# Kernel tuning notes

Measured on AMD Instinct MI355X. Metric: run time of the kernel, lower is better.

## Reference

```python
import jax, jax.numpy as jnp
import numpy as np

N = 2048
E = 512
H = 8
DH = E // H
L = 2
MAX_DIST = 10
LOCAL_DIST = 2
NUM_COLORS = 16
NEG_INF = -1e9


def _layer_norm(x, scale, bias, eps=1e-5):
    mu = jnp.mean(x, axis=-1, keepdims=True)
    var = jnp.mean(jnp.square(x - mu), axis=-1, keepdims=True)
    return (x - mu) * jax.lax.rsqrt(var + eps) * scale + bias


def setup_inputs() -> dict:
    key = jax.random.key(0)
    ks = jax.random.split(key, 12)
    s = 0.05  # weight init scale for numerical sanity
    return {
        "D": jax.random.randint(ks[0], (N, N), 0, MAX_DIST + 2, dtype=jnp.int32),
        "x": jax.random.normal(ks[1], (1, N, E), dtype=jnp.float32),
        "dist_emb": jax.random.normal(ks[2], (MAX_DIST + 2, 8), dtype=jnp.float32) * s,
        "dist_proj_w": jax.random.normal(ks[3], (1, 8), dtype=jnp.float32) * s,
        "dist_proj_b": jnp.zeros((1,), jnp.float32),
        "ln1_scale": jnp.ones((L, E), jnp.float32),
        "ln1_bias": jnp.zeros((L, E), jnp.float32),
        "in_proj_w": jax.random.normal(ks[4], (L, 3 * E, E), dtype=jnp.float32) * s,
        "in_proj_b": jnp.zeros((L, 3 * E), jnp.float32),
        "out_w": jax.random.normal(ks[5], (L, E, E), dtype=jnp.float32) * s,
        "out_b": jnp.zeros((L, E), jnp.float32),
        "ln2_scale": jnp.ones((L, E), jnp.float32),
        "ln2_bias": jnp.zeros((L, E), jnp.float32),
        "ff1_w": jax.random.normal(ks[6], (L, 2 * E, E), dtype=jnp.float32) * s,
        "ff1_b": jnp.zeros((L, 2 * E), jnp.float32),
        "ff2_w": jax.random.normal(ks[7], (L, E, 2 * E), dtype=jnp.float32) * s,
        "ff2_b": jnp.zeros((L, E), jnp.float32),
        "color_w": jax.random.normal(ks[8], (NUM_COLORS, E), dtype=jnp.float32) * s,
        "color_b": jnp.zeros((NUM_COLORS,), jnp.float32),
    }


def reference(D, x, dist_emb, dist_proj_w, dist_proj_b,
              ln1_scale, ln1_bias, in_proj_w, in_proj_b, out_w, out_b,
              ln2_scale, ln2_bias, ff1_w, ff1_b, ff2_w, ff2_b,
              color_w, color_b):
    # Distance encoder: clamp -> embed -> project to scalar bias per (i, j)
    d_clamped = jnp.clip(D, 0, MAX_DIST + 1)                        # [N, N]
    emb = dist_emb[d_clamped]                                       # [N, N, 8]
    bias = jnp.einsum('nme,e->nm', emb, dist_proj_w[0]) + dist_proj_b[0]
    # Graph-local sparsity: real bias within local_dist, -inf elsewhere
    attn_mask = jnp.where(D <= LOCAL_DIST, bias, NEG_INF)           # [N, N]

    scale = 1.0 / jnp.sqrt(jnp.asarray(DH, x.dtype))
    for l in range(L):
        # --- pre-norm multihead self-attention ---
        xn = _layer_norm(x, ln1_scale[l], ln1_bias[l])              # [1, N, E]
        qkv = jnp.einsum('bne,fe->bnf', xn, in_proj_w[l]) + in_proj_b[l]
        q, k, v = jnp.split(qkv, 3, axis=-1)                        # each [1, N, E]
        q = q.reshape(1, N, H, DH)
        k = k.reshape(1, N, H, DH)
        v = v.reshape(1, N, H, DH)
        scores = jnp.einsum('bnhd,bmhd->bhnm', q, k) * scale        # [1, H, N, N]
        scores = scores + attn_mask[None, None, :, :]
        probs = jax.nn.softmax(scores, axis=-1)
        attn = jnp.einsum('bhnm,bmhd->bnhd', probs, v).reshape(1, N, E)
        attn = jnp.einsum('bne,fe->bnf', attn, out_w[l]) + out_b[l]
        x = x + attn                                                # dropout = identity (eval)
        # --- pre-norm feed-forward ---
        xf = _layer_norm(x, ln2_scale[l], ln2_bias[l])
        h = jax.nn.relu(jnp.einsum('bne,fe->bnf', xf, ff1_w[l]) + ff1_b[l])
        ff = jnp.einsum('bnf,ef->bne', h, ff2_w[l]) + ff2_b[l]
        x = x + ff

    logits = jnp.einsum('bne,ce->bnc', x, color_w) + color_b        # [1, N, C]
    return jax.nn.softmax(logits, axis=-1)[0]                       # [N, C]
```

## Files before the change

kernel.cpp:

```cpp
#include <hip/hip_runtime.h>
#include <cstddef>
#include <cstdint>

#define NN 2048
#define EE 512
#define HH 8
#define QKVF 1536
#define NSEG 4

typedef __attribute__((ext_vector_type(4))) float f32x4;
typedef __attribute__((ext_vector_type(8))) short s16x8;
typedef __attribute__((ext_vector_type(4))) short s16x4;

static __device__ __forceinline__ unsigned short f2bf(float x) {
  union { float f; unsigned int u; } c; c.f = x;
  unsigned int r = (c.u + 0x7FFFu + ((c.u >> 16) & 1u)) >> 16;
  return (unsigned short)r;
}
static __device__ __forceinline__ float bf2f(unsigned short b) {
  union { unsigned int u; float f; } c; c.u = ((unsigned int)b) << 16;
  return c.f;
}

#define GLL16(gp, lp) __builtin_amdgcn_global_load_lds( \
    (const __attribute__((address_space(1))) void*)(gp), \
    (__attribute__((address_space(3))) void*)(lp), 16, 0, 0)

__global__ __launch_bounds__(256) void cvt_bf4(const float* __restrict__ src,
    unsigned short* __restrict__ dst, int n4) {
  int i = blockIdx.x * 256 + threadIdx.x;
  if (i < n4) {
    float4 v = ((const float4*)src)[i];
    s16x4 o;
    o[0] = (short)f2bf(v.x); o[1] = (short)f2bf(v.y);
    o[2] = (short)f2bf(v.z); o[3] = (short)f2bf(v.w);
    ((s16x4*)dst)[i] = o;
  }
}

__global__ void wtbl_kernel(const float* __restrict__ demb, const float* __restrict__ dpw,
    const float* __restrict__ dpb, float* __restrict__ wtbl) {
  int t = threadIdx.x;
  if (t < 4) {
    float v = 0.f;
    if (t < 3) {
      float s = 0.f;
      for (int e = 0; e < 8; e++) s += demb[t * 8 + e] * dpw[e];
      v = expf(s + dpb[0]);
    }
    wtbl[t] = v;
  }
}

__global__ __launch_bounds__(256) void mask_pack(const int* __restrict__ D,
    unsigned int* __restrict__ codes) {
  int id = blockIdx.x * 256 + threadIdx.x;
  int row = id >> 9;
  int u = id & 511;
  int ch = u >> 4, col = u & 15;
  int base = ch * 64 + col;
  unsigned int pk = 0;
#pragma unroll
  for (int i = 0; i < 4; i++) {
    int d = D[(size_t)row * NN + base + 16 * i];
    unsigned int c = (d <= 2) ? (unsigned int)d : 3u;
    pk |= c << (8 * i);
  }
  codes[id] = pk;
}

__global__ __launch_bounds__(256) void ln_kernel(const float* __restrict__ x,
    const float* __restrict__ scale, const float* __restrict__ bias,
    unsigned short* __restrict__ out) {
  int row = blockIdx.x;
  int t = threadIdx.x;
  const float* xr = x + (size_t)row * EE;
  float a = xr[t], b = xr[t + 256];
  float s = a + b, q = a * a + b * b;
#pragma unroll
  for (int m = 1; m < 64; m <<= 1) {
    s += __shfl_xor(s, m);
    q += __shfl_xor(q, m);
  }
  __shared__ float ps[4], pq[4];
  int w = t >> 6;
  if ((t & 63) == 0) { ps[w] = s; pq[w] = q; }
  __syncthreads();
  s = ps[0] + ps[1] + ps[2] + ps[3];
  q = pq[0] + pq[1] + pq[2] + pq[3];
  float mu = s * (1.f / EE);
  float var = q * (1.f / EE) - mu * mu;
  float r = rsqrtf(var + 1e-5f);
  unsigned short* orow = out + (size_t)row * EE;
  orow[t] = f2bf((a - mu) * r * scale[t] + bias[t]);
  orow[t + 256] = f2bf((b - mu) * r * scale[t + 256] + bias[t + 256]);
}

template <int RELU, int RES, int OBF>
__global__ __launch_bounds__(256) void gemm_bf(
    const unsigned short* __restrict__ A, const unsigned short* __restrict__ B,
    const float* __restrict__ bias, const float* __restrict__ R,
    void* __restrict__ Cout, int M, int F, int K) {
  __shared__ __attribute__((aligned(16))) unsigned short Al[128 * 64];
  __shared__ __attribute__((aligned(16))) unsigned short Bl[64 * 64];
  const int t = threadIdx.x;
  const int w = t >> 6, l = t & 63;
  const int fr = l & 15, fs = l >> 4;
  const int bm = blockIdx.y * 128, bf = blockIdx.x * 64;
  const int srow = l >> 3, slot = l & 7;
  f32x4 acc[2][4];
  f32x4 zero = {0.f, 0.f, 0.f, 0.f};
#pragma unroll
  for (int i = 0; i < 2; i++)
#pragma unroll
    for (int j = 0; j < 4; j++) acc[i][j] = zero;

  for (int k0 = 0; k0 < K; k0 += 64) {
    __syncthreads();
#pragma unroll
    for (int rnd = 0; rnd < 4; rnd++) {
      int rowblk = w * 4 + rnd;
      int row = rowblk * 8 + srow;
      int koff = (slot * 8) ^ ((row & 7) * 8);
      GLL16(A + (size_t)(bm + row) * K + k0 + koff, Al + rowblk * 512);
    }
#pragma unroll
    for (int rnd = 0; rnd < 2; rnd++) {
      int rowblk = w * 2 + rnd;
      int row = rowblk * 8 + srow;
      int koff = (slot * 8) ^ ((row & 7) * 8);
      GLL16(B + (size_t)(bf + row) * K + k0 + koff, Bl + rowblk * 512);
    }
    __syncthreads();
    s16x8 af[2][2], bg[4][2];
#pragma unroll
    for (int mi = 0; mi < 2; mi++)
#pragma unroll
      for (int ks = 0; ks < 2; ks++) {
        int row = w * 32 + 16 * mi + fr;
        af[mi][ks] = *(const s16x8*)&Al[row * 64 + ((ks * 32 + fs * 8) ^ ((row & 7) * 8))];
      }
#pragma unroll
    for (int ni = 0; ni < 4; ni++)
#pragma unroll
      for (int ks = 0; ks < 2; ks++) {
        int row = 16 * ni + fr;
        bg[ni][ks] = *(const s16x8*)&Bl[row * 64 + ((ks * 32 + fs * 8) ^ ((row & 7) * 8))];
      }
#pragma unroll
    for (int mi = 0; mi < 2; mi++)
#pragma unroll
      for (int ni = 0; ni < 4; ni++)
#pragma unroll
        for (int ks = 0; ks < 2; ks++)
          acc[mi][ni] = __builtin_amdgcn_mfma_f32_16x16x32_bf16(
              af[mi][ks], bg[ni][ks], acc[mi][ni], 0, 0, 0);
  }
#pragma unroll
  for (int mi = 0; mi < 2; mi++)
#pragma unroll
    for (int ni = 0; ni < 4; ni++) {
      int gcol = bf + 16 * ni + fr;
      float bb = bias[gcol];
#pragma unroll
      for (int r = 0; r < 4; r++) {
        int grow = bm + w * 32 + 16 * mi + fs * 4 + r;
        float v = acc[mi][ni][r] + bb;
        if (RELU) v = fmaxf(v, 0.f);
        if (RES) v += R[(size_t)grow * F + gcol];
        if (OBF) ((unsigned short*)Cout)[(size_t)grow * F + gcol] = f2bf(v);
        else ((float*)Cout)[(size_t)grow * F + gcol] = v;
      }
    }
}

__global__ __launch_bounds__(256) void attn_mfma(
    const unsigned short* __restrict__ qkv, const unsigned int* __restrict__ codes,
    const float* __restrict__ wtbl, float* __restrict__ po, float* __restrict__ lpart) {
  __shared__ __attribute__((aligned(16))) unsigned short Kl[64 * 64];
  __shared__ __attribute__((aligned(16))) unsigned short Vt[64 * 64];
  __shared__ __attribute__((aligned(16))) unsigned short Pl[4][16 * 64];
  const int t = threadIdx.x;
  const int w = t >> 6, l = t & 63;
  const int fr = l & 15, fs = l >> 4;
  const int h = blockIdx.y;
  const int seg = blockIdx.z;
  const int qrow0 = blockIdx.x * 64 + w * 16;
  const int kvbase = seg * (NN / NSEG);
  const float C2 = 0.18033688011112042f;

  s16x8 qf[2];
#pragma unroll
  for (int ks = 0; ks < 2; ks++)
    qf[ks] = *(const s16x8*)&qkv[(size_t)(qrow0 + fr) * QKVF + h * 64 + ks * 32 + fs * 8];

  const float w0 = wtbl[0], w1 = wtbl[1], w2 = wtbl[2];

  f32x4 o[4];
  float lacc[4];
  f32x4 zero = {0.f, 0.f, 0.f, 0.f};
#pragma unroll
  for (int i = 0; i < 4; i++) { o[i] = zero; lacc[i] = 0.f; }

  const int krow = t >> 2, kc = (t & 3) * 16;
  const int vkv = (t & 15) * 4, vd = (t >> 4) * 4;
  const unsigned short* kbase = qkv + EE + h * 64;
  const unsigned short* vbase = qkv + 2 * EE + h * 64;
  s16x8 kreg[2];
  s16x4 vreg[4];
#pragma unroll
  for (int i = 0; i < 2; i++)
    kreg[i] = *(const s16x8*)&kbase[(size_t)(kvbase + krow) * QKVF + kc + i * 8];
#pragma unroll
  for (int i = 0; i < 4; i++)
    vreg[i] = *(const s16x4*)&vbase[(size_t)(kvbase + vkv + i) * QKVF + vd];

  for (int ch = 0; ch < NN / NSEG / 64; ch++) {
    __syncthreads();
#pragma unroll
    for (int i = 0; i < 2; i++)
      *(s16x8*)&Kl[krow * 64 + ((kc + i * 8) ^ ((krow & 7) * 8))] = kreg[i];
#pragma unroll
    for (int dj = 0; dj < 4; dj++) {
      int d = vd + dj;
      s16x4 pk;
      pk[0] = vreg[0][dj]; pk[1] = vreg[1][dj]; pk[2] = vreg[2][dj]; pk[3] = vreg[3][dj];
      *(s16x4*)&Vt[d * 64 + (vkv ^ ((d & 7) * 8))] = pk;
    }
    __syncthreads();
    if (ch + 1 < NN / NSEG / 64) {
      int kv0 = kvbase + (ch + 1) * 64;
#pragma unroll
      for (int i = 0; i < 2; i++)
        kreg[i] = *(const s16x8*)&kbase[(size_t)(kv0 + krow) * QKVF + kc + i * 8];
#pragma unroll
      for (int i = 0; i < 4; i++)
        vreg[i] = *(const s16x4*)&vbase[(size_t)(kv0 + vkv + i) * QKVF + vd];
    }
    int gc = kvbase / 64 + ch;
    unsigned int cd[4];
#pragma unroll
    for (int r = 0; r < 4; r++)
      cd[r] = codes[(size_t)(qrow0 + fs * 4 + r) * (NN / 4) + gc * 16 + fr];

    f32x4 s[4];
#pragma unroll
    for (int ni = 0; ni < 4; ni++) s[ni] = zero;
#pragma unroll
    for (int ni = 0; ni < 4; ni++) {
      int row = 16 * ni + fr;
#pragma unroll
      for (int ks = 0; ks < 2; ks++) {
        s16x8 kf = *(const s16x8*)&Kl[row * 64 + ((ks * 32 + fs * 8) ^ ((row & 7) * 8))];
        s[ni] = __builtin_amdgcn_mfma_f32_16x16x32_bf16(qf[ks], kf, s[ni], 0, 0, 0);
      }
    }
#pragma unroll
    for (int r = 0; r < 4; r++) {
      int prow = fs * 4 + r;
      float psum = 0.f;
#pragma unroll
      for (int ni = 0; ni < 4; ni++) {
        unsigned int code = (cd[r] >> (8 * ni)) & 255u;
        float wsel = code == 0u ? w0 : (code == 1u ? w1 : (code == 2u ? w2 : 0.f));
        float p = exp2f(s[ni][r] * C2) * wsel;
        unsigned short pb = f2bf(p);
        psum += bf2f(pb);
        Pl[w][prow * 64 + ((16 * ni + fr) ^ ((prow & 7) * 8))] = pb;
      }
      lacc[r] += psum;
    }
#pragma unroll
    for (int ks = 0; ks < 2; ks++) {
      s16x8 pa = *(const s16x8*)&Pl[w][fr * 64 + ((ks * 32 + fs * 8) ^ ((fr & 7) * 8))];
#pragma unroll
      for (int dn = 0; dn < 4; dn++) {
        int row = 16 * dn + fr;
        s16x8 vf = *(const s16x8*)&Vt[row * 64 + ((ks * 32 + fs * 8) ^ ((row & 7) * 8))];
        o[dn] = __builtin_amdgcn_mfma_f32_16x16x32_bf16(pa, vf, o[dn], 0, 0, 0);
      }
    }
  }
#pragma unroll
  for (int r = 0; r < 4; r++) {
#pragma unroll
    for (int m = 1; m < 16; m <<= 1) lacc[r] += __shfl_xor(lacc[r], m);
  }
#pragma unroll
  for (int r = 0; r < 4; r++) {
    int row = qrow0 + fs * 4 + r;
#pragma unroll
    for (int dn = 0; dn < 4; dn++)
      po[((size_t)seg * NN + row) * EE + h * 64 + 16 * dn + fr] = o[dn][r];
    if (fr == 0) lpart[((size_t)seg * NN + row) * 8 + h] = lacc[r];
  }
}

__global__ __launch_bounds__(256) void attn_combine(const float* __restrict__ po,
    const float* __restrict__ lpart, unsigned short* __restrict__ attnb) {
  int id = blockIdx.x * 256 + threadIdx.x;
  int row = id >> 7;
  int col = (id & 127) * 4;
  int h = col >> 6;
  float4 o = {0.f, 0.f, 0.f, 0.f};
  float lsum = 0.f;
#pragma unroll
  for (int s = 0; s < NSEG; s++) {
    float4 p4 = *(const float4*)&po[((size_t)s * NN + row) * EE + col];
    o.x += p4.x; o.y += p4.y; o.z += p4.z; o.w += p4.w;
    lsum += lpart[((size_t)s * NN + row) * 8 + h];
  }
  float inv = 1.f / lsum;
  s16x4 ob;
  ob[0] = (short)f2bf(o.x * inv); ob[1] = (short)f2bf(o.y * inv);
  ob[2] = (short)f2bf(o.z * inv); ob[3] = (short)f2bf(o.w * inv);
  *(s16x4*)&attnb[(size_t)row * EE + col] = ob;
}

__global__ __launch_bounds__(256) void logits_kernel(const float* __restrict__ x,
    const float* __restrict__ cw, const float* __restrict__ cb,
    float* __restrict__ out) {
  int t = threadIdx.x;
  int wv = t >> 6, lane = t & 63;
  int row = blockIdx.x * 4 + wv;
  const float* xr = x + (size_t)row * EE;
  int c = lane >> 2, p = lane & 3;
  const float* w = cw + c * EE;
  float s = 0.f;
  for (int e = p * 128; e < p * 128 + 128; e++) s += xr[e] * w[e];
  s += __shfl_xor(s, 1);
  s += __shfl_xor(s, 2);
  __shared__ float lg[4][16];
  if (p == 0) lg[wv][c] = s + cb[c];
  __syncthreads();
  if (lane < 16) {
    float mx = -INFINITY;
#pragma unroll
    for (int k = 0; k < 16; k++) mx = fmaxf(mx, lg[wv][k]);
    float sum = 0.f;
#pragma unroll
    for (int k = 0; k < 16; k++) sum += __expf(lg[wv][k] - mx);
    out[(size_t)row * 16 + lane] = __expf(lg[wv][lane] - mx) / sum;
  }
}

extern "C" void kernel_launch(void* const* d_in, const int* in_sizes, int n_in,
                              void* d_out, int out_size, void* d_ws, size_t ws_size,
                              hipStream_t stream) {
  const int* D = (const int*)d_in[0];
  const float* x = (const float*)d_in[1];
  const float* demb = (const float*)d_in[2];
  const float* dpw = (const float*)d_in[3];
  const float* dpb = (const float*)d_in[4];
  const float* ln1s = (const float*)d_in[5];
  const float* ln1b = (const float*)d_in[6];
  const float* ipw = (const float*)d_in[7];
  const float* ipb = (const float*)d_in[8];
  const float* ow = (const float*)d_in[9];
  const float* ob = (const float*)d_in[10];
  const float* ln2s = (const float*)d_in[11];
  const float* ln2b = (const float*)d_in[12];
  const float* f1w = (const float*)d_in[13];
  const float* f1b = (const float*)d_in[14];
  const float* f2w = (const float*)d_in[15];
  const float* f2b = (const float*)d_in[16];
  const float* cw = (const float*)d_in[17];
  const float* cb = (const float*)d_in[18];

  char* base = (char*)d_ws;
  unsigned int* codes = (unsigned int*)base;
  float* xbuf = (float*)(base + (4u << 20));
  unsigned short* qkv = (unsigned short*)(base + (8u << 20));
  unsigned short* xn = (unsigned short*)(base + (14u << 20));
  unsigned short* attnb = (unsigned short*)(base + (16u << 20));
  unsigned short* hbuf = (unsigned short*)(base + (18u << 20));
  unsigned short* ipw_bf = (unsigned short*)(base + (22u << 20));
  unsigned short* ow_bf = (unsigned short*)(base + (25u << 20));
  unsigned short* f1w_bf = (unsigned short*)(base + (26u << 20));
  unsigned short* f2w_bf = (unsigned short*)(base + (28u << 20));
  float* wtbl = (float*)(base + (30u << 20));
  float* po = (float*)(base + (31u << 20));
  float* lpart = (float*)(base + (47u << 20));

  cvt_bf4<<<(393216 + 255) / 256, 256, 0, stream>>>(ipw, ipw_bf, 393216);
  cvt_bf4<<<(131072 + 255) / 256, 256, 0, stream>>>(ow, ow_bf, 131072);
  cvt_bf4<<<(262144 + 255) / 256, 256, 0, stream>>>(f1w, f1w_bf, 262144);
  cvt_bf4<<<(262144 + 255) / 256, 256, 0, stream>>>(f2w, f2w_bf, 262144);
  wtbl_kernel<<<1, 64, 0, stream>>>(demb, dpw, dpb, wtbl);
  mask_pack<<<4096, 256, 0, stream>>>(D, codes);
  hipMemcpyAsync(xbuf, x, (size_t)NN * EE * sizeof(float), hipMemcpyDeviceToDevice, stream);

  for (int l = 0; l < 2; l++) {
    ln_kernel<<<NN, 256, 0, stream>>>(xbuf, ln1s + l * EE, ln1b + l * EE, xn);
    gemm_bf<0, 0, 1><<<dim3(24, 16), 256, 0, stream>>>(
        xn, ipw_bf + (size_t)l * 786432, ipb + l * 1536, nullptr, qkv, NN, 1536, 512);
    attn_mfma<<<dim3(32, HH, NSEG), 256, 0, stream>>>(qkv, codes, wtbl, po, lpart);
    attn_combine<<<1024, 256, 0, stream>>>(po, lpart, attnb);
    gemm_bf<0, 1, 0><<<dim3(8, 16), 256, 0, stream>>>(
        attnb, ow_bf + (size_t)l * 262144, ob + l * EE, xbuf, xbuf, NN, 512, 512);
    ln_kernel<<<NN, 256, 0, stream>>>(xbuf, ln2s + l * EE, ln2b + l * EE, xn);
    gemm_bf<1, 0, 1><<<dim3(16, 16), 256, 0, stream>>>(
        xn, f1w_bf + (size_t)l * 524288, f1b + l * 1024, nullptr, hbuf, NN, 1024, 512);
    gemm_bf<0, 1, 0><<<dim3(8, 16), 256, 0, stream>>>(
        hbuf, f2w_bf + (size_t)l * 524288, f2b + l * EE, xbuf, xbuf, NN, 512, 1024);
  }
  logits_kernel<<<NN / 4, 256, 0, stream>>>(xbuf, cw, cb, (float*)d_out);
}
```

Measured before the change: 324.4 us.

## Double-buffer GEMM with smaller tiles, fuse setup kernels, drop x copy

```diff
diff --git a/kernel.cpp b/kernel.cpp
--- a/kernel.cpp
+++ b/kernel.cpp
@@ -26,30 +26,29 @@
     (const __attribute__((address_space(1))) void*)(gp), \
     (__attribute__((address_space(3))) void*)(lp), 16, 0, 0)
 
-__global__ __launch_bounds__(256) void cvt_bf4(const float* __restrict__ src,
-    unsigned short* __restrict__ dst, int n4) {
-  int i = blockIdx.x * 256 + threadIdx.x;
-  if (i < n4) {
-    float4 v = ((const float4*)src)[i];
-    s16x4 o;
-    o[0] = (short)f2bf(v.x); o[1] = (short)f2bf(v.y);
-    o[2] = (short)f2bf(v.z); o[3] = (short)f2bf(v.w);
-    ((s16x4*)dst)[i] = o;
-  }
-}
-
-__global__ void wtbl_kernel(const float* __restrict__ demb, const float* __restrict__ dpw,
-    const float* __restrict__ dpb, float* __restrict__ wtbl) {
-  int t = threadIdx.x;
-  if (t < 4) {
-    float v = 0.f;
-    if (t < 3) {
-      float s = 0.f;
-      for (int e = 0; e < 8; e++) s += demb[t * 8 + e] * dpw[e];
-      v = expf(s + dpb[0]);
-    }
-    wtbl[t] = v;
-  }
+__global__ __launch_bounds__(256) void cvt_all(
+    const float* __restrict__ s0, const float* __restrict__ s1,
+    const float* __restrict__ s2, const float* __restrict__ s3,
+    unsigned short* __restrict__ d0, unsigned short* __restrict__ d1,
+    unsigned short* __restrict__ d2, unsigned short* __restrict__ d3,
+    int n0, int n1, int n2, int n3) {
+  int j = blockIdx.x * 256 + threadIdx.x;
+  const float* s; unsigned short* d;
+  if (j < n0) { s = s0; d = d0; }
+  else {
+    j -= n0;
+    if (j < n1) { s = s1; d = d1; }
+    else {
+      j -= n1;
+      if (j < n2) { s = s2; d = d2; }
+      else { j -= n2; if (j >= n3) return; s = s3; d = d3; }
+    }
+  }
+  float4 v = ((const float4*)s)[j];
+  s16x4 o;
+  o[0] = (short)f2bf(v.x); o[1] = (short)f2bf(v.y);
+  o[2] = (short)f2bf(v.z); o[3] = (short)f2bf(v.w);
+  ((s16x4*)d)[j] = o;
 }
 
 __global__ __launch_bounds__(256) void mask_pack(const int* __restrict__ D,
@@ -101,82 +100,77 @@
     const unsigned short* __restrict__ A, const unsigned short* __restrict__ B,
     const float* __restrict__ bias, const float* __restrict__ R,
     void* __restrict__ Cout, int M, int F, int K) {
-  __shared__ __attribute__((aligned(16))) unsigned short Al[128 * 64];
-  __shared__ __attribute__((aligned(16))) unsigned short Bl[64 * 64];
+  __shared__ __attribute__((aligned(16))) unsigned short Al[2][64 * 64];
+  __shared__ __attribute__((aligned(16))) unsigned short Bl[2][64 * 64];
   const int t = threadIdx.x;
   const int w = t >> 6, l = t & 63;
   const int fr = l & 15, fs = l >> 4;
-  const int bm = blockIdx.y * 128, bf = blockIdx.x * 64;
+  const int bm = blockIdx.y * 64, bf = blockIdx.x * 64;
   const int srow = l >> 3, slot = l & 7;
-  f32x4 acc[2][4];
+  const int nk = K >> 6;
+
+  f32x4 acc[4];
   f32x4 zero = {0.f, 0.f, 0.f, 0.f};
 #pragma unroll
-  for (int i = 0; i < 2; i++)
-#pragma unroll
-    for (int j = 0; j < 4; j++) acc[i][j] = zero;
-
-  for (int k0 = 0; k0 < K; k0 += 64) {
-    __syncthreads();
-#pragma unroll
-    for (int rnd = 0; rnd < 4; rnd++) {
-      int rowblk = w * 4 + rnd;
-      int row = rowblk * 8 + srow;
-      int koff = (slot * 8) ^ ((row & 7) * 8);
-      GLL16(A + (size_t)(bm + row) * K + k0 + koff, Al + rowblk * 512);
-    }
+  for (int j = 0; j < 4; j++) acc[j] = zero;
+
+  auto stage = [&](int kt, int bsel) {
+    int k0 = kt * 64;
 #pragma unroll
     for (int rnd = 0; rnd < 2; rnd++) {
       int rowblk = w * 2 + rnd;
       int row = rowblk * 8 + srow;
       int koff = (slot * 8) ^ ((row & 7) * 8);
-      GLL16(B + (size_t)(bf + row) * K + k0 + koff, Bl + rowblk * 512);
-    }
-    __syncthreads();
-    s16x8 af[2][2], bg[4][2];
-#pragma unroll
-    for (int mi = 0; mi < 2; mi++)
-#pragma unroll
-      for (int ks = 0; ks < 2; ks++) {
-        int row = w * 32 + 16 * mi + fr;
-        af[mi][ks] = *(const s16x8*)&Al[row * 64 + ((ks * 32 + fs * 8) ^ ((row & 7) * 8))];
-      }
+      GLL16(A + (size_t)(bm + row) * K + k0 + koff, &Al[bsel][rowblk * 512]);
+      GLL16(B + (size_t)(bf + row) * K + k0 + koff, &Bl[bsel][rowblk * 512]);
+    }
+  };
+
+  stage(0, 0);
+  __syncthreads();
+  for (int kt = 0; kt < nk; kt++) {
+    const int cur = kt & 1;
+    if (kt + 1 < nk) stage(kt + 1, cur ^ 1);
+    s16x8 af[2], bg[4][2];
+    const int arow = w * 16 + fr;
+#pragma unroll
+    for (int ks = 0; ks < 2; ks++)
+      af[ks] = *(const s16x8*)&Al[cur][arow * 64 + ((ks * 32 + fs * 8) ^ ((arow & 7) * 8))];
 #pragma unroll
     for (int ni = 0; ni < 4; ni++)
 #pragma unroll
       for (int ks = 0; ks < 2; ks++) {
         int row = 16 * ni + fr;
-        bg[ni][ks] = *(const s16x8*)&Bl[row * 64 + ((ks * 32 + fs * 8) ^ ((row & 7) * 8))];
+        bg[ni][ks] = *(const s16x8*)&Bl[cur][row * 64 + ((ks * 32 + fs * 8) ^ ((row & 7) * 8))];
       }
 #pragma unroll
-    for (int mi = 0; mi < 2; mi++)
-#pragma unroll
-      for (int ni = 0; ni < 4; ni++)
-#pragma unroll
-        for (int ks = 0; ks < 2; ks++)
-          acc[mi][ni] = __builtin_amdgcn_mfma_f32_16x16x32_bf16(
-              af[mi][ks], bg[ni][ks], acc[mi][ni], 0, 0, 0);
-  }
-#pragma unroll
-  for (int mi = 0; mi < 2; mi++)
-#pragma unroll
-    for (int ni = 0; ni < 4; ni++) {
-      int gcol = bf + 16 * ni + fr;
-      float bb = bias[gcol];
-#pragma unroll
-      for (int r = 0; r < 4; r++) {
-        int grow = bm + w * 32 + 16 * mi + fs * 4 + r;
-        float v = acc[mi][ni][r] + bb;
-        if (RELU) v = fmaxf(v, 0.f);
-        if (RES) v += R[(size_t)grow * F + gcol];
-        if (OBF) ((unsigned short*)Cout)[(size_t)grow * F + gcol] = f2bf(v);
-        else ((float*)Cout)[(size_t)grow * F + gcol] = v;
-      }
-    }
+    for (int ni = 0; ni < 4; ni++)
+#pragma unroll
+      for (int ks = 0; ks < 2; ks++)
+        acc[ni] = __builtin_amdgcn_mfma_f32_16x16x32_bf16(af[ks], bg[ni][ks], acc[ni], 0, 0, 0);
+    __syncthreads();
+  }
+
+#pragma unroll
+  for (int ni = 0; ni < 4; ni++) {
+    int gcol = bf + 16 * ni + fr;
+    float bb = bias[gcol];
+#pragma unroll
+    for (int r = 0; r < 4; r++) {
+      int grow = bm + w * 16 + fs * 4 + r;
+      float v = acc[ni][r] + bb;
+      if (RELU) v = fmaxf(v, 0.f);
+      if (RES) v += R[(size_t)grow * F + gcol];
+      if (OBF) ((unsigned short*)Cout)[(size_t)grow * F + gcol] = f2bf(v);
+      else ((float*)Cout)[(size_t)grow * F + gcol] = v;
+    }
+  }
 }
 
 __global__ __launch_bounds__(256) void attn_mfma(
     const unsigned short* __restrict__ qkv, const unsigned int* __restrict__ codes,
-    const float* __restrict__ wtbl, float* __restrict__ po, float* __restrict__ lpart) {
+    const float* __restrict__ demb, const float* __restrict__ dpw,
+    const float* __restrict__ dpb, float* __restrict__ po, float* __restrict__ lpart) {
   __shared__ __attribute__((aligned(16))) unsigned short Kl[64 * 64];
   __shared__ __attribute__((aligned(16))) unsigned short Vt[64 * 64];
   __shared__ __attribute__((aligned(16))) unsigned short Pl[4][16 * 64];
@@ -189,12 +183,22 @@
   const int kvbase = seg * (NN / NSEG);
   const float C2 = 0.18033688011112042f;
 
+  float w0, w1, w2;
+  {
+    float s0 = 0.f, s1 = 0.f, s2 = 0.f;
+#pragma unroll
+    for (int e = 0; e < 8; e++) {
+      float pw = dpw[e];
+      s0 += demb[e] * pw; s1 += demb[8 + e] * pw; s2 += demb[16 + e] * pw;
+    }
+    float b = dpb[0];
+    w0 = __expf(s0 + b); w1 = __expf(s1 + b); w2 = __expf(s2 + b);
+  }
+
   s16x8 qf[2];
 #pragma unroll
   for (int ks = 0; ks < 2; ks++)
     qf[ks] = *(const s16x8*)&qkv[(size_t)(qrow0 + fr) * QKVF + h * 64 + ks * 32 + fs * 8];
-
-  const float w0 = wtbl[0], w1 = wtbl[1], w2 = wtbl[2];
 
   f32x4 o[4];
   float lacc[4];
@@ -246,6 +250,7 @@
     f32x4 s[4];
 #pragma unroll
     for (int ni = 0; ni < 4; ni++) s[ni] = zero;
+    __builtin_amdgcn_s_setprio(1);
 #pragma unroll
     for (int ni = 0; ni < 4; ni++) {
       int row = 16 * ni + fr;
@@ -255,6 +260,7 @@
         s[ni] = __builtin_amdgcn_mfma_f32_16x16x32_bf16(qf[ks], kf, s[ni], 0, 0, 0);
       }
     }
+    __builtin_amdgcn_s_setprio(0);
 #pragma unroll
     for (int r = 0; r < 4; r++) {
       int prow = fs * 4 + r;
@@ -270,6 +276,7 @@
       }
       lacc[r] += psum;
     }
+    __builtin_amdgcn_s_setprio(1);
 #pragma unroll
     for (int ks = 0; ks < 2; ks++) {
       s16x8 pa = *(const s16x8*)&Pl[w][fr * 64 + ((ks * 32 + fs * 8) ^ ((fr & 7) * 8))];
@@ -280,6 +287,7 @@
         o[dn] = __builtin_amdgcn_mfma_f32_16x16x32_bf16(pa, vf, o[dn], 0, 0, 0);
       }
     }
+    __builtin_amdgcn_s_setprio(0);
   }
 #pragma unroll
   for (int r = 0; r < 4; r++) {
@@ -378,30 +386,26 @@
   unsigned short* ow_bf = (unsigned short*)(base + (25u << 20));
   unsigned short* f1w_bf = (unsigned short*)(base + (26u << 20));
   unsigned short* f2w_bf = (unsigned short*)(base + (28u << 20));
-  float* wtbl = (float*)(base + (30u << 20));
   float* po = (float*)(base + (31u << 20));
   float* lpart = (float*)(base + (47u << 20));
 
-  cvt_bf4<<<(393216 + 255) / 256, 256, 0, stream>>>(ipw, ipw_bf, 393216);
-  cvt_bf4<<<(131072 + 255) / 256, 256, 0, stream>>>(ow, ow_bf, 131072);
-  cvt_bf4<<<(262144 + 255) / 256, 256, 0, stream>>>(f1w, f1w_bf, 262144);
-  cvt_bf4<<<(262144 + 255) / 256, 256, 0, stream>>>(f2w, f2w_bf, 262144);
-  wtbl_kernel<<<1, 64, 0, stream>>>(demb, dpw, dpb, wtbl);
+  cvt_all<<<4096, 256, 0, stream>>>(ipw, ow, f1w, f2w,
+      ipw_bf, ow_bf, f1w_bf, f2w_bf, 393216, 131072, 262144, 262144);
   mask_pack<<<4096, 256, 0, stream>>>(D, codes);
-  hipMemcpyAsync(xbuf, x, (size_t)NN * EE * sizeof(float), hipMemcpyDeviceToDevice, stream);
 
   for (int l = 0; l < 2; l++) {
-    ln_kernel<<<NN, 256, 0, stream>>>(xbuf, ln1s + l * EE, ln1b + l * EE, xn);
-    gemm_bf<0, 0, 1><<<dim3(24, 16), 256, 0, stream>>>(
+    const float* xin = (l == 0) ? x : xbuf;
+    ln_kernel<<<NN, 256, 0, stream>>>(xin, ln1s + l * EE, ln1b + l * EE, xn);
+    gemm_bf<0, 0, 1><<<dim3(24, 32), 256, 0, stream>>>(
         xn, ipw_bf + (size_t)l * 786432, ipb + l * 1536, nullptr, qkv, NN, 1536, 512);
-    attn_mfma<<<dim3(32, HH, NSEG), 256, 0, stream>>>(qkv, codes, wtbl, po, lpart);
+    attn_mfma<<<dim3(32, HH, NSEG), 256, 0, stream>>>(qkv, codes, demb, dpw, dpb, po, lpart);
     attn_combine<<<1024, 256, 0, stream>>>(po, lpart, attnb);
-    gemm_bf<0, 1, 0><<<dim3(8, 16), 256, 0, stream>>>(
-        attnb, ow_bf + (size_t)l * 262144, ob + l * EE, xbuf, xbuf, NN, 512, 512);
+    gemm_bf<0, 1, 0><<<dim3(8, 32), 256, 0, stream>>>(
+        attnb, ow_bf + (size_t)l * 262144, ob + l * EE, xin, xbuf, NN, 512, 512);
     ln_kernel<<<NN, 256, 0, stream>>>(xbuf, ln2s + l * EE, ln2b + l * EE, xn);
-    gemm_bf<1, 0, 1><<<dim3(16, 16), 256, 0, stream>>>(
+    gemm_bf<1, 0, 1><<<dim3(16, 32), 256, 0, stream>>>(
         xn, f1w_bf + (size_t)l * 524288, f1b + l * 1024, nullptr, hbuf, NN, 1024, 512);
-    gemm_bf<0, 1, 0><<<dim3(8, 16), 256, 0, stream>>>(
+    gemm_bf<0, 1, 0><<<dim3(8, 32), 256, 0, stream>>>(
         hbuf, f2w_bf + (size_t)l * 524288, f2b + l * EE, xbuf, xbuf, NN, 512, 1024);
   }
   logits_kernel<<<NN / 4, 256, 0, stream>>>(xbuf, cw, cb, (float*)d_out);
```

New measurement: 316.0 us. -2.6%, faster.
